# Optimization experiments

Hardware: AMD Instinct MI355X
Metric: run time of the kernel (lower is better)

## Reference

```python
import math
import jax, jax.numpy as jnp
import numpy as np

NUM_HEADS = 12
KEEP_RATE = 0.7


def setup_inputs() -> dict:
    key = jax.random.key(0)
    k1, k2, k3 = jax.random.split(key, 3)
    B, N, C = 16, 577, 768
    x = jax.random.normal(k1, (B, N, C), dtype=jnp.float32)
    qkv_w = jax.random.normal(k2, (3 * C, C), dtype=jnp.float32) * 0.02
    proj_w = jax.random.normal(k3, (C, C), dtype=jnp.float32) * 0.02
    proj_b = jnp.zeros((C,), dtype=jnp.float32)
    return {"x": x, "qkv_w": qkv_w, "proj_w": proj_w, "proj_b": proj_b}


def reference(x, qkv_w, proj_w, proj_b):
    B, N, C = x.shape
    H = NUM_HEADS
    hd = C // H
    scale = hd ** -0.5
    # qkv projection (no bias): [B, N, 3C] -> [3, B, H, N, hd]
    qkv = (x @ qkv_w.T).reshape(B, N, 3, H, hd).transpose(2, 0, 3, 1, 4)
    q, k, v = qkv[0], qkv[1], qkv[2]
    attn = jax.nn.softmax(jnp.einsum('bhnd,bhmd->bhnm', q, k) * scale, axis=-1)
    out = jnp.einsum('bhnm,bhmd->bhnd', attn, v)          # [B,H,N,hd]
    out = out.transpose(0, 2, 1, 3).reshape(B, N, C)
    out = out @ proj_w.T + proj_b
    # CLS-token attention pruning (keep_rate < 1.0, return_idx=True path)
    left_tokens = math.ceil(KEEP_RATE * (N - 1))
    cls_attn = attn[:, :, 0, 1:].mean(axis=1)             # [B, N-1], mean over heads
    _, idx = jax.lax.top_k(cls_attn, left_tokens)         # sorted descending
    index = jnp.broadcast_to(idx[:, :, None], (B, left_tokens, C))
    return out, idx, index, cls_attn
```

## Files before the change

### kernel.cpp

```cpp
#include <hip/hip_runtime.h>
#include <math.h>

#define BB 16
#define NN 577
#define CC 768
#define HH 12
#define HD 64
#define MM (BB*NN)
#define MPAD 9344
#define LEFT 404
#define NPAD 608
#define NQT 10

typedef __attribute__((ext_vector_type(8))) short short8v;
typedef __attribute__((ext_vector_type(4))) float f32x4;

__device__ __forceinline__ unsigned short f2bf(float f) {
    union { float f; unsigned int u; } v; v.f = f;
    unsigned int r = v.u + 0x7fffu + ((v.u >> 16) & 1u);
    return (unsigned short)(r >> 16);
}

__device__ __forceinline__ short8v cvt8(float4 lo, float4 hi) {
    short8v r;
    r[0]=(short)f2bf(lo.x); r[1]=(short)f2bf(lo.y); r[2]=(short)f2bf(lo.z); r[3]=(short)f2bf(lo.w);
    r[4]=(short)f2bf(hi.x); r[5]=(short)f2bf(hi.y); r[6]=(short)f2bf(hi.z); r[7]=(short)f2bf(hi.w);
    return r;
}

__global__ __launch_bounds__(256) void k_gemm_fp32(const float* __restrict__ X,
                                                   const float* __restrict__ W,
                                                   float* __restrict__ kb,
                                                   unsigned short* __restrict__ kbh)
{
    __shared__ float Xs[16][128];
    __shared__ float Ws[16][128];
    const int t  = threadIdx.x;
    const int tx = t & 15, ty = t >> 4;
    const int m0 = blockIdx.x * 128;
    const int n0 = 768 + blockIdx.y * 128;
    const int sm = t & 127;
    const int sk = (t >> 7) * 8;

    float acc[8][8];
    #pragma unroll
    for (int i = 0; i < 8; ++i)
        #pragma unroll
        for (int j = 0; j < 8; ++j) acc[i][j] = 0.f;

    const int gm = m0 + sm;
    const float* px = X + (size_t)gm * CC + sk;
    const float* pw = W + (size_t)(n0 + sm) * CC + sk;

    float4 a0 = make_float4(0.f,0.f,0.f,0.f), a1 = a0, b0, b1;
    if (gm < MM) { a0 = *(const float4*)px; a1 = *(const float4*)(px + 4); }
    b0 = *(const float4*)pw; b1 = *(const float4*)(pw + 4);

    for (int kk = 0; kk < CC; kk += 16) {
        Xs[sk+0][sm] = a0.x; Xs[sk+1][sm] = a0.y; Xs[sk+2][sm] = a0.z; Xs[sk+3][sm] = a0.w;
        Xs[sk+4][sm] = a1.x; Xs[sk+5][sm] = a1.y; Xs[sk+6][sm] = a1.z; Xs[sk+7][sm] = a1.w;
        Ws[sk+0][sm] = b0.x; Ws[sk+1][sm] = b0.y; Ws[sk+2][sm] = b0.z; Ws[sk+3][sm] = b0.w;
        Ws[sk+4][sm] = b1.x; Ws[sk+5][sm] = b1.y; Ws[sk+6][sm] = b1.z; Ws[sk+7][sm] = b1.w;
        __syncthreads();
        if (kk + 16 < CC) {
            a0 = make_float4(0.f,0.f,0.f,0.f); a1 = a0;
            if (gm < MM) { a0 = *(const float4*)(px + kk + 16); a1 = *(const float4*)(px + kk + 20); }
            b0 = *(const float4*)(pw + kk + 16); b1 = *(const float4*)(pw + kk + 20);
        }
        #pragma unroll
        for (int k = 0; k < 16; ++k) {
            float a[8], bv[8];
            *(float4*)&a[0]  = *(const float4*)&Xs[k][ty*4];
            *(float4*)&a[4]  = *(const float4*)&Xs[k][64 + ty*4];
            *(float4*)&bv[0] = *(const float4*)&Ws[k][tx*4];
            *(float4*)&bv[4] = *(const float4*)&Ws[k][64 + tx*4];
            #pragma unroll
            for (int i = 0; i < 8; ++i)
                #pragma unroll
                for (int j = 0; j < 8; ++j)
                    acc[i][j] = fmaf(a[i], bv[j], acc[i][j]);
        }
        __syncthreads();
    }
    #pragma unroll
    for (int i = 0; i < 8; ++i) {
        const int mrow = m0 + ((i < 4) ? (ty*4 + i) : (64 + ty*4 + i - 4));
        if (mrow >= MM) continue;
        const int b_ = mrow / NN;
        const int n_ = mrow - b_ * NN;
        #pragma unroll
        for (int j = 0; j < 8; ++j) {
            const int col = (n0 - 768) + ((j < 4) ? (tx*4 + j) : (64 + tx*4 + j - 4));
            const int h = col >> 6, d = col & 63;
            const float a = acc[i][j];
            kb [(((size_t)b_ * HH + h) * NN   + n_) * HD + d] = a;
            kbh[(((size_t)b_ * HH + h) * NPAD + n_) * HD + d] = f2bf(a);
        }
    }
}

__global__ __launch_bounds__(256) void qcls_kernel(const float* __restrict__ X,
                                                   const float* __restrict__ W,
                                                   float* __restrict__ qcls)
{
    const int b = blockIdx.x;
    const int col = blockIdx.y * 256 + threadIdx.x;
    const float* xr = X + (size_t)b * NN * CC;
    const float* wr = W + (size_t)col * CC;
    float acc = 0.f;
    for (int k = 0; k < CC; ++k) acc = fmaf(xr[k], wr[k], acc);
    qcls[(size_t)b * CC + col] = acc;
}

#define N4W 442368
#define N4P 147456
__global__ __launch_bounds__(256) void convert_w(const float* __restrict__ wq,
                                                 const float* __restrict__ wp,
                                                 unsigned short* __restrict__ wqb,
                                                 unsigned short* __restrict__ wpb)
{
    int g = blockIdx.x * 256 + threadIdx.x;
    const float* src; unsigned short* dst;
    if (g < N4W)            { src = wq; dst = wqb; }
    else                    { g -= N4W; src = wp; dst = wpb; }
    const float4 v = ((const float4*)src)[g];
    ushort4 o;
    o.x = f2bf(v.x); o.y = f2bf(v.y); o.z = f2bf(v.z); o.w = f2bf(v.w);
    ((ushort4*)dst)[g] = o;
}

__global__ __launch_bounds__(256) void qv_mfma(const float* __restrict__ X,
                                               const unsigned short* __restrict__ wqkv,
                                               unsigned short* __restrict__ qbh,
                                               unsigned short* __restrict__ Vt)
{
    __shared__ unsigned short As[128*32];
    __shared__ unsigned short Bs[128*32];
    const int t = threadIdx.x;
    const int w = t >> 6, l = t & 63;
    const int l15 = l & 15, lk = l >> 4;
    const int wm = w >> 1, wn = w & 1;
    const int m0 = blockIdx.x * 128;
    const int isV = blockIdx.y >= 6;
    const int nlocal0 = (isV ? (blockIdx.y - 6) : blockIdx.y) * 128;
    const int wrow0 = (isV ? 1536 : 0) + nlocal0;
    const int r0 = t >> 2, segp = t & 3;

    f32x4 acc[4][4];
    #pragma unroll
    for (int i = 0; i < 4; ++i)
        #pragma unroll
        for (int j = 0; j < 4; ++j) acc[i][j] = (f32x4){0.f,0.f,0.f,0.f};

    const int gr0 = (m0 + r0      < MM) ? (m0 + r0)      : 0;
    const int gr1 = (m0 + 64 + r0 < MM) ? (m0 + 64 + r0) : 0;
    const float* ga0 = X + (size_t)gr0 * CC + segp * 8;
    const float* ga1 = X + (size_t)gr1 * CC + segp * 8;
    const unsigned short* gb = wqkv + (size_t)(wrow0 + r0) * CC + segp * 8;

    for (int kk = 0; kk < CC; kk += 32) {
        const float4 f00 = *(const float4*)(ga0 + kk);
        const float4 f01 = *(const float4*)(ga0 + kk + 4);
        const float4 f10 = *(const float4*)(ga1 + kk);
        const float4 f11 = *(const float4*)(ga1 + kk + 4);
        const short8v b0 = *(const short8v*)(gb + kk);
        const short8v b1 = *(const short8v*)(gb + kk + (size_t)64 * CC);
        const short8v a0 = cvt8(f00, f01);
        const short8v a1 = cvt8(f10, f11);
        __syncthreads();
        *(short8v*)&As[(r0)      * 32 + segp*8] = a0;
        *(short8v*)&As[(64 + r0) * 32 + segp*8] = a1;
        *(short8v*)&Bs[(r0)      * 32 + segp*8] = b0;
        *(short8v*)&Bs[(64 + r0) * 32 + segp*8] = b1;
        __syncthreads();
        short8v fa[4], fb[4];
        #pragma unroll
        for (int i = 0; i < 4; ++i) fa[i] = *(const short8v*)&As[(wm*64 + i*16 + l15)*32 + lk*8];
        #pragma unroll
        for (int j = 0; j < 4; ++j) fb[j] = *(const short8v*)&Bs[(wn*64 + j*16 + l15)*32 + lk*8];
        #pragma unroll
        for (int i = 0; i < 4; ++i)
            #pragma unroll
            for (int j = 0; j < 4; ++j)
                acc[i][j] = __builtin_amdgcn_mfma_f32_16x16x32_bf16(fa[i], fb[j], acc[i][j], 0, 0, 0);
    }

    const int nb = nlocal0 + wn*64 + l15;
    #pragma unroll
    for (int i = 0; i < 4; ++i) {
        #pragma unroll
        for (int r = 0; r < 4; ++r) {
            const int m = m0 + wm*64 + i*16 + 4*lk + r;
            if (m >= MM) continue;
            const int b_ = m / NN, tok = m - b_ * NN;
            #pragma unroll
            for (int j = 0; j < 4; ++j) {
                const int nl = nb + j*16;
                const int h = nl >> 6, d = nl & 63;
                const unsigned short v = f2bf(acc[i][j][r]);
                if (isV) Vt [(((size_t)b_*HH + h)*HD + d)*NPAD + tok] = v;
                else     qbh[(((size_t)b_*HH + h)*NPAD + tok)*HD + d] = v;
            }
        }
    }
}

__global__ __launch_bounds__(256) void proj_mfma(const unsigned short* __restrict__ aobh,
                                                 const unsigned short* __restrict__ wpb,
                                                 const float* __restrict__ bias,
                                                 float* __restrict__ outp)
{
    __shared__ unsigned short As[128*32];
    __shared__ unsigned short Bs[128*32];
    const int t = threadIdx.x;
    const int w = t >> 6, l = t & 63;
    const int l15 = l & 15, lk = l >> 4;
    const int wm = w >> 1, wn = w & 1;
    const int m0 = blockIdx.x * 128;
    const int n0 = blockIdx.y * 128;
    const int r0 = t >> 2, segp = t & 3;

    f32x4 acc[4][4];
    #pragma unroll
    for (int i = 0; i < 4; ++i)
        #pragma unroll
        for (int j = 0; j < 4; ++j) acc[i][j] = (f32x4){0.f,0.f,0.f,0.f};

    const unsigned short* ga = aobh + (size_t)(m0 + r0) * CC + segp * 8;
    const unsigned short* gb = wpb  + (size_t)(n0 + r0) * CC + segp * 8;

    for (int kk = 0; kk < CC; kk += 32) {
        const short8v a0 = *(const short8v*)(ga + kk);
        const short8v a1 = *(const short8v*)(ga + kk + (size_t)64 * CC);
        const short8v b0 = *(const short8v*)(gb + kk);
        const short8v b1 = *(const short8v*)(gb + kk + (size_t)64 * CC);
        __syncthreads();
        *(short8v*)&As[(r0)      * 32 + segp*8] = a0;
        *(short8v*)&As[(64 + r0) * 32 + segp*8] = a1;
        *(short8v*)&Bs[(r0)      * 32 + segp*8] = b0;
        *(short8v*)&Bs[(64 + r0) * 32 + segp*8] = b1;
        __syncthreads();
        short8v fa[4], fb[4];
        #pragma unroll
        for (int i = 0; i < 4; ++i) fa[i] = *(const short8v*)&As[(wm*64 + i*16 + l15)*32 + lk*8];
        #pragma unroll
        for (int j = 0; j < 4; ++j) fb[j] = *(const short8v*)&Bs[(wn*64 + j*16 + l15)*32 + lk*8];
        #pragma unroll
        for (int i = 0; i < 4; ++i)
            #pragma unroll
            for (int j = 0; j < 4; ++j)
                acc[i][j] = __builtin_amdgcn_mfma_f32_16x16x32_bf16(fa[i], fb[j], acc[i][j], 0, 0, 0);
    }

    const int nb = n0 + wn*64 + l15;
    #pragma unroll
    for (int i = 0; i < 4; ++i) {
        #pragma unroll
        for (int r = 0; r < 4; ++r) {
            const int m = m0 + wm*64 + i*16 + 4*lk + r;
            if (m >= MM) continue;
            #pragma unroll
            for (int j = 0; j < 4; ++j) {
                const int n = nb + j*16;
                outp[(size_t)m * CC + n] = acc[i][j][r] + bias[n];
            }
        }
    }
}

__global__ __launch_bounds__(256) void attn_mfma(const unsigned short* __restrict__ qbh,
                                                 const unsigned short* __restrict__ kbh,
                                                 const unsigned short* __restrict__ Vt,
                                                 unsigned short* __restrict__ aobh)
{
    __shared__ __align__(16) unsigned short plds[4][16][32];
    const int bid = blockIdx.x;
    const int bh  = bid / NQT;
    const int qt  = bid - bh * NQT;
    const int b   = bh / HH, h = bh - b * HH;
    const int t   = threadIdx.x;
    const int w   = t >> 6, l = t & 63;
    const int l15 = l & 15, lg = l >> 4;

    short8v aq0, aq1;
    {
        int qrow = qt*64 + w*16 + l15; if (qrow > 576) qrow = 576;
        const unsigned short* qp = qbh + ((size_t)bh * NPAD + qrow) * HD + lg*8;
        aq0 = *(const short8v*)(qp);
        aq1 = *(const short8v*)(qp + 32);
    }

    f32x4 O0 = {0.f,0.f,0.f,0.f}, O1 = O0, O2 = O0, O3 = O0;
    float mr[4] = {-1e30f,-1e30f,-1e30f,-1e30f};
    float lr[4] = {0.f,0.f,0.f,0.f};

    const unsigned short* kwb = kbh + (size_t)bh * NPAD * HD + (size_t)l15 * HD + lg*8;
    const unsigned short* vwb = Vt  + (size_t)bh * HD * NPAD + (size_t)l15 * NPAD + lg*8;

    for (int c = 0; c < 19; ++c) {
        const int n0 = c * 32;
        const unsigned short* kp = kwb + (size_t)n0 * HD;
        short8v bk00 = *(const short8v*)(kp);
        short8v bk01 = *(const short8v*)(kp + 32);
        short8v bk10 = *(const short8v*)(kp + 16*HD);
        short8v bk11 = *(const short8v*)(kp + 16*HD + 32);
        f32x4 s0 = {0.f,0.f,0.f,0.f}, s1 = {0.f,0.f,0.f,0.f};
        s0 = __builtin_amdgcn_mfma_f32_16x16x32_bf16(aq0, bk00, s0, 0, 0, 0);
        s0 = __builtin_amdgcn_mfma_f32_16x16x32_bf16(aq1, bk01, s0, 0, 0, 0);
        s1 = __builtin_amdgcn_mfma_f32_16x16x32_bf16(aq0, bk10, s1, 0, 0, 0);
        s1 = __builtin_amdgcn_mfma_f32_16x16x32_bf16(aq1, bk11, s1, 0, 0, 0);

        const int nc0 = n0 + l15;
        float p0[4], p1[4], al[4];
        #pragma unroll
        for (int r = 0; r < 4; ++r) {
            float a0 = (nc0      <= 576) ? s0[r] * 0.125f : -1e30f;
            float a1 = (nc0 + 16 <= 576) ? s1[r] * 0.125f : -1e30f;
            float tm = fmaxf(a0, a1);
            tm = fmaxf(tm, __shfl_xor(tm, 1, 64));
            tm = fmaxf(tm, __shfl_xor(tm, 2, 64));
            tm = fmaxf(tm, __shfl_xor(tm, 4, 64));
            tm = fmaxf(tm, __shfl_xor(tm, 8, 64));
            const float mn = fmaxf(mr[r], tm);
            al[r] = __expf(mr[r] - mn);
            mr[r] = mn;
            p0[r] = __expf(a0 - mn);
            p1[r] = __expf(a1 - mn);
            float ps = p0[r] + p1[r];
            ps += __shfl_xor(ps, 1, 64);
            ps += __shfl_xor(ps, 2, 64);
            ps += __shfl_xor(ps, 4, 64);
            ps += __shfl_xor(ps, 8, 64);
            lr[r] = lr[r] * al[r] + ps;
        }
        #pragma unroll
        for (int r = 0; r < 4; ++r) {
            O0[r] *= al[r]; O1[r] *= al[r]; O2[r] *= al[r]; O3[r] *= al[r];
        }
        #pragma unroll
        for (int r = 0; r < 4; ++r) {
            plds[w][lg*4 + r][l15]      = f2bf(p0[r]);
            plds[w][lg*4 + r][16 + l15] = f2bf(p1[r]);
        }
        asm volatile("s_waitcnt lgkmcnt(0)" ::: "memory");
        short8v pa = *(const short8v*)&plds[w][l15][lg*8];
        const unsigned short* vp = vwb + n0;
        short8v v0 = *(const short8v*)(vp);
        short8v v1 = *(const short8v*)(vp + 16*NPAD);
        short8v v2 = *(const short8v*)(vp + 32*NPAD);
        short8v v3 = *(const short8v*)(vp + 48*NPAD);
        O0 = __builtin_amdgcn_mfma_f32_16x16x32_bf16(pa, v0, O0, 0, 0, 0);
        O1 = __builtin_amdgcn_mfma_f32_16x16x32_bf16(pa, v1, O1, 0, 0, 0);
        O2 = __builtin_amdgcn_mfma_f32_16x16x32_bf16(pa, v2, O2, 0, 0, 0);
        O3 = __builtin_amdgcn_mfma_f32_16x16x32_bf16(pa, v3, O3, 0, 0, 0);
    }

    #pragma unroll
    for (int r = 0; r < 4; ++r) {
        const float inv = 1.f / lr[r];
        const int row = qt*64 + w*16 + lg*4 + r;
        if (row <= 576) {
            unsigned short* op = aobh + ((size_t)b * NN + row) * CC + h*HD + l15;
            op[0]  = f2bf(O0[r] * inv);
            op[16] = f2bf(O1[r] * inv);
            op[32] = f2bf(O2[r] * inv);
            op[48] = f2bf(O3[r] * inv);
        }
    }
}

__global__ __launch_bounds__(256) void cls_scores(const float* __restrict__ qcls,
                                                  const float* __restrict__ kb,
                                                  float* __restrict__ P)
{
    const int bh = blockIdx.x;
    const int t = threadIdx.x;
    __shared__ float q[64];
    __shared__ float red[256];
    __shared__ float L[NN];
    if (t < 64) q[t] = qcls[(size_t)bh * 64 + t];
    __syncthreads();
    float lmax = -1e30f;
    for (int n = t; n < NN; n += 256) {
        const float* kr = kb + ((size_t)bh * NN + n) * HD;
        float acc = 0.f;
        #pragma unroll
        for (int d = 0; d < 64; ++d) acc = fmaf(q[d], kr[d], acc);
        const float l = acc * 0.125f;
        L[n] = l;
        lmax = fmaxf(lmax, l);
    }
    red[t] = lmax; __syncthreads();
    for (int s = 128; s > 0; s >>= 1) { if (t < s) red[t] = fmaxf(red[t], red[t+s]); __syncthreads(); }
    const float m = red[0]; __syncthreads();
    float z = 0.f;
    for (int n = t; n < NN; n += 256) { const float e = expf(L[n] - m); L[n] = e; z += e; }
    red[t] = z; __syncthreads();
    for (int s = 128; s > 0; s >>= 1) { if (t < s) red[t] += red[t+s]; __syncthreads(); }
    const float Z = red[0];
    for (int n = t; n < NN; n += 256) P[(size_t)bh * NN + n] = L[n] / Z;
}

__global__ __launch_bounds__(256) void cls_meantopk(const float* __restrict__ P,
                                                    float* __restrict__ out_cls,
                                                    float* __restrict__ out_idx,
                                                    int* __restrict__ idxi)
{
    const int b = blockIdx.x;
    const int t = threadIdx.x;
    __shared__ float sv[576];
    for (int j = t; j < 576; j += 256) {
        float s = 0.f;
        #pragma unroll
        for (int h = 0; h < HH; ++h) s += P[((size_t)(b * HH + h)) * NN + 1 + j];
        const float v = s / 12.0f;
        sv[j] = v;
        out_cls[b * 576 + j] = v;
    }
    __syncthreads();
    for (int i = t; i < 576; i += 256) {
        const float vi = sv[i];
        int rank = 0;
        for (int j = 0; j < 576; ++j) {
            const float vj = sv[j];
            if (vj > vi || (vj == vi && j < i)) ++rank;
        }
        if (rank < LEFT) {
            out_idx[(size_t)b * LEFT + rank] = (float)i;
            idxi[(size_t)b * LEFT + rank] = i;
        }
    }
}

__global__ void write_index(const int* __restrict__ idxi, float* __restrict__ out_index)
{
    const int g4 = blockIdx.x * 256 + threadIdx.x;
    const float v = (float)idxi[g4 / 192];
    float4 o; o.x = v; o.y = v; o.z = v; o.w = v;
    ((float4*)out_index)[g4] = o;
}

extern "C" void kernel_launch(void* const* d_in, const int* in_sizes, int n_in,
                              void* d_out, int out_size, void* d_ws, size_t ws_size,
                              hipStream_t stream)
{
    const float* x      = (const float*)d_in[0];
    const float* qkv_w  = (const float*)d_in[1];
    const float* proj_w = (const float*)d_in[2];
    const float* proj_b = (const float*)d_in[3];
    float* out = (float*)d_out;

    char* base = (char*)d_ws;
    float*          kb    = (float*)(base + 0);
    unsigned short* qbh   = (unsigned short*)(base +  42713088);
    unsigned short* kbh   = (unsigned short*)(base +  57655296);
    unsigned short* Vt    = (unsigned short*)(base +  72597504);
    unsigned short* aobh  = (unsigned short*)(base +  87539712);
    unsigned short* wqkv  = (unsigned short*)(base + 101892096);
    unsigned short* wpb   = (unsigned short*)(base + 105431040);
    float*          qcls  = (float*)(base + 106610688);
    float*          P     = (float*)(base + 106659840);
    int*            idxi  = (int*)  (base + 107139840);

    float* out_main  = out;
    float* out_idx   = out + 7090176;
    float* out_index = out + 7096640;
    float* out_cls   = out + 12060992;

    convert_w<<<2304, 256, 0, stream>>>(qkv_w, proj_w, wqkv, wpb);
    qcls_kernel<<<dim3(16, 3), 256, 0, stream>>>(x, qkv_w, qcls);
    k_gemm_fp32<<<dim3(73, 6), 256, 0, stream>>>(x, qkv_w, kb, kbh);
    qv_mfma<<<dim3(73, 12), 256, 0, stream>>>(x, wqkv, qbh, Vt);
    attn_mfma<<<BB * HH * NQT, 256, 0, stream>>>(qbh, kbh, Vt, aobh);
    proj_mfma<<<dim3(73, 6), 256, 0, stream>>>(aobh, wpb, proj_b, out_main);

    cls_scores<<<BB * HH, 256, 0, stream>>>(qcls, kb, P);
    cls_meantopk<<<BB, 256, 0, stream>>>(P, out_cls, out_idx, idxi);
    write_index<<<4848, 256, 0, stream>>>(idxi, out_index);
}
```

Baseline: 452.4 us.

## Double-buffer LDS in FP32 K GEMM and split CLS scoring into logits and softmax

The FP32 K-projection GEMM now keeps two shared-memory stages, so the next tile is written while the current one is consumed, leaving one barrier per iteration instead of two. Separately, the CLS score kernel is split in two: a logits kernel spread over three times as many blocks, and a separate softmax kernel over the stored logits. This is meant to hide global-load latency in the GEMM and to add parallelism to the small CLS path. The cost is double the LDS in the GEMM, which may lower occupancy, plus one extra kernel launch and an extra pass over global memory for the logits.

```diff
diff --git a/kernel.cpp b/kernel.cpp
--- a/kernel.cpp
+++ b/kernel.cpp
@@ -33,8 +33,8 @@
                                                    float* __restrict__ kb,
                                                    unsigned short* __restrict__ kbh)
 {
-    __shared__ float Xs[16][128];
-    __shared__ float Ws[16][128];
+    __shared__ float Xs[2][16][128];
+    __shared__ float Ws[2][16][128];
     const int t  = threadIdx.x;
     const int tx = t & 15, ty = t >> 4;
     const int m0 = blockIdx.x * 128;
@@ -52,36 +52,52 @@
     const float* px = X + (size_t)gm * CC + sk;
     const float* pw = W + (size_t)(n0 + sm) * CC + sk;
 
-    float4 a0 = make_float4(0.f,0.f,0.f,0.f), a1 = a0, b0, b1;
-    if (gm < MM) { a0 = *(const float4*)px; a1 = *(const float4*)(px + 4); }
-    b0 = *(const float4*)pw; b1 = *(const float4*)(pw + 4);
-
+    {
+        float4 a0 = make_float4(0.f,0.f,0.f,0.f), a1 = a0;
+        if (gm < MM) { a0 = *(const float4*)px; a1 = *(const float4*)(px + 4); }
+        float4 b0 = *(const float4*)pw;
+        float4 b1 = *(const float4*)(pw + 4);
+        Xs[0][sk+0][sm] = a0.x; Xs[0][sk+1][sm] = a0.y; Xs[0][sk+2][sm] = a0.z; Xs[0][sk+3][sm] = a0.w;
+        Xs[0][sk+4][sm] = a1.x; Xs[0][sk+5][sm] = a1.y; Xs[0][sk+6][sm] = a1.z; Xs[0][sk+7][sm] = a1.w;
+        Ws[0][sk+0][sm] = b0.x; Ws[0][sk+1][sm] = b0.y; Ws[0][sk+2][sm] = b0.z; Ws[0][sk+3][sm] = b0.w;
+        Ws[0][sk+4][sm] = b1.x; Ws[0][sk+5][sm] = b1.y; Ws[0][sk+6][sm] = b1.z; Ws[0][sk+7][sm] = b1.w;
+    }
+    __syncthreads();
+
+    int cur = 0;
     for (int kk = 0; kk < CC; kk += 16) {
-        Xs[sk+0][sm] = a0.x; Xs[sk+1][sm] = a0.y; Xs[sk+2][sm] = a0.z; Xs[sk+3][sm] = a0.w;
-        Xs[sk+4][sm] = a1.x; Xs[sk+5][sm] = a1.y; Xs[sk+6][sm] = a1.z; Xs[sk+7][sm] = a1.w;
-        Ws[sk+0][sm] = b0.x; Ws[sk+1][sm] = b0.y; Ws[sk+2][sm] = b0.z; Ws[sk+3][sm] = b0.w;
-        Ws[sk+4][sm] = b1.x; Ws[sk+5][sm] = b1.y; Ws[sk+6][sm] = b1.z; Ws[sk+7][sm] = b1.w;
-        __syncthreads();
-        if (kk + 16 < CC) {
+        float4 a0, a1, b0, b1;
+        const bool more = (kk + 16 < CC);
+        if (more) {
             a0 = make_float4(0.f,0.f,0.f,0.f); a1 = a0;
             if (gm < MM) { a0 = *(const float4*)(px + kk + 16); a1 = *(const float4*)(px + kk + 20); }
-            b0 = *(const float4*)(pw + kk + 16); b1 = *(const float4*)(pw + kk + 20);
+            b0 = *(const float4*)(pw + kk + 16);
+            b1 = *(const float4*)(pw + kk + 20);
         }
         #pragma unroll
         for (int k = 0; k < 16; ++k) {
             float a[8], bv[8];
-            *(float4*)&a[0]  = *(const float4*)&Xs[k][ty*4];
-            *(float4*)&a[4]  = *(const float4*)&Xs[k][64 + ty*4];
-            *(float4*)&bv[0] = *(const float4*)&Ws[k][tx*4];
-            *(float4*)&bv[4] = *(const float4*)&Ws[k][64 + tx*4];
+            *(float4*)&a[0]  = *(const float4*)&Xs[cur][k][ty*4];
+            *(float4*)&a[4]  = *(const float4*)&Xs[cur][k][64 + ty*4];
+            *(float4*)&bv[0] = *(const float4*)&Ws[cur][k][tx*4];
+            *(float4*)&bv[4] = *(const float4*)&Ws[cur][k][64 + tx*4];
             #pragma unroll
             for (int i = 0; i < 8; ++i)
                 #pragma unroll
                 for (int j = 0; j < 8; ++j)
                     acc[i][j] = fmaf(a[i], bv[j], acc[i][j]);
         }
+        if (more) {
+            const int nx = cur ^ 1;
+            Xs[nx][sk+0][sm] = a0.x; Xs[nx][sk+1][sm] = a0.y; Xs[nx][sk+2][sm] = a0.z; Xs[nx][sk+3][sm] = a0.w;
+            Xs[nx][sk+4][sm] = a1.x; Xs[nx][sk+5][sm] = a1.y; Xs[nx][sk+6][sm] = a1.z; Xs[nx][sk+7][sm] = a1.w;
+            Ws[nx][sk+0][sm] = b0.x; Ws[nx][sk+1][sm] = b0.y; Ws[nx][sk+2][sm] = b0.z; Ws[nx][sk+3][sm] = b0.w;
+            Ws[nx][sk+4][sm] = b1.x; Ws[nx][sk+5][sm] = b1.y; Ws[nx][sk+6][sm] = b1.z; Ws[nx][sk+7][sm] = b1.w;
+        }
         __syncthreads();
-    }
+        cur ^= 1;
+    }
+
     #pragma unroll
     for (int i = 0; i < 8; ++i) {
         const int mrow = m0 + ((i < 4) ? (ty*4 + i) : (64 + ty*4 + i - 4));
@@ -369,36 +385,42 @@
     }
 }
 
-__global__ __launch_bounds__(256) void cls_scores(const float* __restrict__ qcls,
+__global__ __launch_bounds__(256) void cls_logits(const float* __restrict__ qcls,
                                                   const float* __restrict__ kb,
                                                   float* __restrict__ P)
 {
     const int bh = blockIdx.x;
     const int t = threadIdx.x;
     __shared__ float q[64];
-    __shared__ float red[256];
-    __shared__ float L[NN];
     if (t < 64) q[t] = qcls[(size_t)bh * 64 + t];
     __syncthreads();
-    float lmax = -1e30f;
-    for (int n = t; n < NN; n += 256) {
+    const int n = blockIdx.y * 193 + t;
+    if (t < 193 && n < NN) {
         const float* kr = kb + ((size_t)bh * NN + n) * HD;
         float acc = 0.f;
         #pragma unroll
         for (int d = 0; d < 64; ++d) acc = fmaf(q[d], kr[d], acc);
-        const float l = acc * 0.125f;
-        L[n] = l;
-        lmax = fmaxf(lmax, l);
-    }
+        P[(size_t)bh * NN + n] = acc * 0.125f;
+    }
+}
+
+__global__ __launch_bounds__(256) void cls_softmax(float* __restrict__ P)
+{
+    const int bh = blockIdx.x;
+    const int t = threadIdx.x;
+    float* L = P + (size_t)bh * NN;
+    __shared__ float red[256];
+    float lmax = -1e30f;
+    for (int n = t; n < NN; n += 256) lmax = fmaxf(lmax, L[n]);
     red[t] = lmax; __syncthreads();
     for (int s = 128; s > 0; s >>= 1) { if (t < s) red[t] = fmaxf(red[t], red[t+s]); __syncthreads(); }
     const float m = red[0]; __syncthreads();
     float z = 0.f;
-    for (int n = t; n < NN; n += 256) { const float e = expf(L[n] - m); L[n] = e; z += e; }
+    for (int n = t; n < NN; n += 256) z += expf(L[n] - m);
     red[t] = z; __syncthreads();
     for (int s = 128; s > 0; s >>= 1) { if (t < s) red[t] += red[t+s]; __syncthreads(); }
     const float Z = red[0];
-    for (int n = t; n < NN; n += 256) P[(size_t)bh * NN + n] = L[n] / Z;
+    for (int n = t; n < NN; n += 256) L[n] = expf(L[n] - m) / Z;
 }
 
 __global__ __launch_bounds__(256) void cls_meantopk(const float* __restrict__ P,
@@ -474,7 +496,8 @@
     attn_mfma<<<BB * HH * NQT, 256, 0, stream>>>(qbh, kbh, Vt, aobh);
     proj_mfma<<<dim3(73, 6), 256, 0, stream>>>(aobh, wpb, proj_b, out_main);
 
-    cls_scores<<<BB * HH, 256, 0, stream>>>(qcls, kb, P);
+    cls_logits<<<dim3(BB * HH, 3), 256, 0, stream>>>(qcls, kb, P);
+    cls_softmax<<<BB * HH, 256, 0, stream>>>(P);
     cls_meantopk<<<BB, 256, 0, stream>>>(P, out_cls, out_idx, idxi);
     write_index<<<4848, 256, 0, stream>>>(idxi, out_index);
 }
```

New measurement: 512.8 us. +13.3%, slower.

## Pre-convert x to bf16 once and split CLS scoring into logits and softmax

Applied to the files above, without the earlier changes.

The activation x is now converted to bf16 in one combined conversion kernel alongside the weights. The Q/V MFMA GEMM then loads bf16 directly, instead of re-reading fp32 x and converting it in each of its 12 column-block passes. This halves the GEMM's A-operand traffic and removes the repeated conversion work, at the cost of an extra pass that reads x and writes the bf16 copy. Separately, the per-head CLS score kernel is split into a wider-grid logits kernel and a separate softmax kernel to get more parallelism. Padding rows beyond the real token count are read from uninitialized workspace, which is only safe if those rows are masked on store.

```diff
diff --git a/kernel.cpp b/kernel.cpp
--- a/kernel.cpp
+++ b/kernel.cpp
@@ -19,13 +19,6 @@
     union { float f; unsigned int u; } v; v.f = f;
     unsigned int r = v.u + 0x7fffu + ((v.u >> 16) & 1u);
     return (unsigned short)(r >> 16);
-}
-
-__device__ __forceinline__ short8v cvt8(float4 lo, float4 hi) {
-    short8v r;
-    r[0]=(short)f2bf(lo.x); r[1]=(short)f2bf(lo.y); r[2]=(short)f2bf(lo.z); r[3]=(short)f2bf(lo.w);
-    r[4]=(short)f2bf(hi.x); r[5]=(short)f2bf(hi.y); r[6]=(short)f2bf(hi.z); r[7]=(short)f2bf(hi.w);
-    return r;
 }
 
 __global__ __launch_bounds__(256) void k_gemm_fp32(const float* __restrict__ X,
@@ -112,24 +105,28 @@
     qcls[(size_t)b * CC + col] = acc;
 }
 
+#define N4X 1772544
 #define N4W 442368
 #define N4P 147456
-__global__ __launch_bounds__(256) void convert_w(const float* __restrict__ wq,
-                                                 const float* __restrict__ wp,
-                                                 unsigned short* __restrict__ wqb,
-                                                 unsigned short* __restrict__ wpb)
+__global__ __launch_bounds__(256) void convert3(const float* __restrict__ x,
+                                                const float* __restrict__ wq,
+                                                const float* __restrict__ wp,
+                                                unsigned short* __restrict__ xb,
+                                                unsigned short* __restrict__ wqb,
+                                                unsigned short* __restrict__ wpb)
 {
     int g = blockIdx.x * 256 + threadIdx.x;
     const float* src; unsigned short* dst;
-    if (g < N4W)            { src = wq; dst = wqb; }
-    else                    { g -= N4W; src = wp; dst = wpb; }
+    if (g < N4X)            { src = x;  dst = xb;  }
+    else if (g < N4X + N4W) { g -= N4X; src = wq; dst = wqb; }
+    else                    { g -= (N4X + N4W); src = wp; dst = wpb; }
     const float4 v = ((const float4*)src)[g];
     ushort4 o;
     o.x = f2bf(v.x); o.y = f2bf(v.y); o.z = f2bf(v.z); o.w = f2bf(v.w);
     ((ushort4*)dst)[g] = o;
 }
 
-__global__ __launch_bounds__(256) void qv_mfma(const float* __restrict__ X,
+__global__ __launch_bounds__(256) void qv_mfma(const unsigned short* __restrict__ xbh,
                                                const unsigned short* __restrict__ wqkv,
                                                unsigned short* __restrict__ qbh,
                                                unsigned short* __restrict__ Vt)
@@ -152,21 +149,14 @@
         #pragma unroll
         for (int j = 0; j < 4; ++j) acc[i][j] = (f32x4){0.f,0.f,0.f,0.f};
 
-    const int gr0 = (m0 + r0      < MM) ? (m0 + r0)      : 0;
-    const int gr1 = (m0 + 64 + r0 < MM) ? (m0 + 64 + r0) : 0;
-    const float* ga0 = X + (size_t)gr0 * CC + segp * 8;
-    const float* ga1 = X + (size_t)gr1 * CC + segp * 8;
+    const unsigned short* ga = xbh  + (size_t)(m0 + r0) * CC + segp * 8;
     const unsigned short* gb = wqkv + (size_t)(wrow0 + r0) * CC + segp * 8;
 
     for (int kk = 0; kk < CC; kk += 32) {
-        const float4 f00 = *(const float4*)(ga0 + kk);
-        const float4 f01 = *(const float4*)(ga0 + kk + 4);
-        const float4 f10 = *(const float4*)(ga1 + kk);
-        const float4 f11 = *(const float4*)(ga1 + kk + 4);
+        const short8v a0 = *(const short8v*)(ga + kk);
+        const short8v a1 = *(const short8v*)(ga + kk + (size_t)64 * CC);
         const short8v b0 = *(const short8v*)(gb + kk);
         const short8v b1 = *(const short8v*)(gb + kk + (size_t)64 * CC);
-        const short8v a0 = cvt8(f00, f01);
-        const short8v a1 = cvt8(f10, f11);
         __syncthreads();
         *(short8v*)&As[(r0)      * 32 + segp*8] = a0;
         *(short8v*)&As[(64 + r0) * 32 + segp*8] = a1;
@@ -369,36 +359,42 @@
     }
 }
 
-__global__ __launch_bounds__(256) void cls_scores(const float* __restrict__ qcls,
+__global__ __launch_bounds__(256) void cls_logits(const float* __restrict__ qcls,
                                                   const float* __restrict__ kb,
                                                   float* __restrict__ P)
 {
     const int bh = blockIdx.x;
     const int t = threadIdx.x;
     __shared__ float q[64];
-    __shared__ float red[256];
-    __shared__ float L[NN];
     if (t < 64) q[t] = qcls[(size_t)bh * 64 + t];
     __syncthreads();
-    float lmax = -1e30f;
-    for (int n = t; n < NN; n += 256) {
+    const int n = blockIdx.y * 193 + t;
+    if (t < 193 && n < NN) {
         const float* kr = kb + ((size_t)bh * NN + n) * HD;
         float acc = 0.f;
         #pragma unroll
         for (int d = 0; d < 64; ++d) acc = fmaf(q[d], kr[d], acc);
-        const float l = acc * 0.125f;
-        L[n] = l;
-        lmax = fmaxf(lmax, l);
-    }
+        P[(size_t)bh * NN + n] = acc * 0.125f;
+    }
+}
+
+__global__ __launch_bounds__(256) void cls_softmax(float* __restrict__ P)
+{
+    const int bh = blockIdx.x;
+    const int t = threadIdx.x;
+    float* L = P + (size_t)bh * NN;
+    __shared__ float red[256];
+    float lmax = -1e30f;
+    for (int n = t; n < NN; n += 256) lmax = fmaxf(lmax, L[n]);
     red[t] = lmax; __syncthreads();
     for (int s = 128; s > 0; s >>= 1) { if (t < s) red[t] = fmaxf(red[t], red[t+s]); __syncthreads(); }
     const float m = red[0]; __syncthreads();
     float z = 0.f;
-    for (int n = t; n < NN; n += 256) { const float e = expf(L[n] - m); L[n] = e; z += e; }
+    for (int n = t; n < NN; n += 256) z += expf(L[n] - m);
     red[t] = z; __syncthreads();
     for (int s = 128; s > 0; s >>= 1) { if (t < s) red[t] += red[t+s]; __syncthreads(); }
     const float Z = red[0];
-    for (int n = t; n < NN; n += 256) P[(size_t)bh * NN + n] = L[n] / Z;
+    for (int n = t; n < NN; n += 256) L[n] = expf(L[n] - m) / Z;
 }
 
 __global__ __launch_bounds__(256) void cls_meantopk(const float* __restrict__ P,
@@ -452,6 +448,7 @@
 
     char* base = (char*)d_ws;
     float*          kb    = (float*)(base + 0);
+    unsigned short* xbh   = (unsigned short*)(base +  28360704);
     unsigned short* qbh   = (unsigned short*)(base +  42713088);
     unsigned short* kbh   = (unsigned short*)(base +  57655296);
     unsigned short* Vt    = (unsigned short*)(base +  72597504);
@@ -467,14 +464,15 @@
     float* out_index = out + 7096640;
     float* out_cls   = out + 12060992;
 
-    convert_w<<<2304, 256, 0, stream>>>(qkv_w, proj_w, wqkv, wpb);
+    convert3<<<9228, 256, 0, stream>>>(x, qkv_w, proj_w, xbh, wqkv, wpb);
     qcls_kernel<<<dim3(16, 3), 256, 0, stream>>>(x, qkv_w, qcls);
     k_gemm_fp32<<<dim3(73, 6), 256, 0, stream>>>(x, qkv_w, kb, kbh);
-    qv_mfma<<<dim3(73, 12), 256, 0, stream>>>(x, wqkv, qbh, Vt);
+    qv_mfma<<<dim3(73, 12), 256, 0, stream>>>(xbh, wqkv, qbh, Vt);
     attn_mfma<<<BB * HH * NQT, 256, 0, stream>>>(qbh, kbh, Vt, aobh);
     proj_mfma<<<dim3(73, 6), 256, 0, stream>>>(aobh, wpb, proj_b, out_main);
 
-    cls_scores<<<BB * HH, 256, 0, stream>>>(qcls, kb, P);
+    cls_logits<<<dim3(BB * HH, 3), 256, 0, stream>>>(qcls, kb, P);
+    cls_softmax<<<BB * HH, 256, 0, stream>>>(P);
     cls_meantopk<<<BB, 256, 0, stream>>>(P, out_cls, out_idx, idxi);
     write_index<<<4848, 256, 0, stream>>>(idxi, out_index);
 }
```

Result: faster. 437.5 us, median of 2 (-3.3%).
